# Kernel optimization log

Hardware: AMD Instinct MI355X
Metric: run time of the kernel (lower is better)

## Reference

```python
import jax, jax.numpy as jnp
import numpy as np
import math

N_STFT = 1025
N_MELS = 128
SAMPLE_RATE = 16000
F_MIN = 0.0
F_MAX = 8000.0
MAX_ITER = 20
LR = 0.3
MOMENTUM = 0.9
BATCH = 4
TIME = 1024


def _create_fb_matrix(n_freqs, f_min, f_max, n_mels, sample_rate):
    # Triangular mel filterbank, (n_freqs, n_mels), matching torchaudio's create_fb_matrix.
    all_freqs = np.linspace(0.0, sample_rate // 2, n_freqs)
    m_min = 2595.0 * math.log10(1.0 + f_min / 700.0)
    m_max = 2595.0 * math.log10(1.0 + f_max / 700.0)
    m_pts = np.linspace(m_min, m_max, n_mels + 2)
    f_pts = 700.0 * (10.0 ** (m_pts / 2595.0) - 1.0)
    f_diff = f_pts[1:] - f_pts[:-1]
    slopes = f_pts[None, :] - all_freqs[:, None]  # (n_freqs, n_mels+2)
    down_slopes = -slopes[:, :-2] / f_diff[:-1]
    up_slopes = slopes[:, 2:] / f_diff[1:]
    fb = np.maximum(0.0, np.minimum(down_slopes, up_slopes))
    return jnp.asarray(fb, dtype=jnp.float32)


def setup_inputs() -> dict:
    key = jax.random.key(0)
    k1, k2 = jax.random.split(key)
    melspec = jax.random.uniform(k1, (BATCH, N_MELS, TIME), dtype=jnp.float32)
    # torch.rand initialization of the estimated spectrogram, exposed for determinism
    spec_init = jax.random.uniform(k2, (BATCH, TIME, N_STFT), dtype=jnp.float32)
    fb = _create_fb_matrix(N_STFT, F_MIN, F_MAX, N_MELS, SAMPLE_RATE)
    return {"melspec": melspec, "spec_init": spec_init, "fb": fb}


def reference(melspec, spec_init, fb):
    # melspec: (B, n_mels, T) -> (B, T, n_mels); fb: (n_stft, n_mels)
    mel_t = jnp.swapaxes(melspec, -1, -2)
    b, t, _ = mel_t.shape
    inv = 2.0 / (b * t)  # d(mean over B*T of sum_m diff^2)/d(spec) prefactor

    def step(carry, _):
        spec, buf = carry
        diff = mel_t - jnp.einsum('btf,fm->btm', spec, fb)      # (B,T,M)
        grad = -inv * jnp.einsum('btm,fm->btf', diff, fb)       # (B,T,F)
        buf = MOMENTUM * buf + grad                              # SGD momentum buffer
        spec = jnp.maximum(spec - LR * buf, 0.0)                 # update + clamp(min=0)
        return (spec, buf), None

    init = (spec_init, jnp.zeros_like(spec_init))
    (spec, _), _ = jax.lax.scan(step, init, None, length=MAX_ITER)
    return jnp.swapaxes(spec, -1, -2)  # (B, n_stft, T)
```

## Files before the change

### kernel.cpp

```cpp
#include <hip/hip_runtime.h>

#define N_STFT 1025
#define N_MELS 128
#define BATCH 4
#define TIME 1024
#define MAX_ITER 20

typedef unsigned int u32;

__global__ void imel_prep(const float* __restrict__ fb, int* __restrict__ m0f,
                          float* __restrict__ w0a, float* __restrict__ w1a) {
  const int w = threadIdx.x >> 6, l = threadIdx.x & 63;
  const int f = blockIdx.x * 4 + w;
  if (f >= N_STFT) return;
  const float* row = fb + (size_t)f * N_MELS;
  const unsigned long long mlo = __ballot(row[l] != 0.0f);
  const unsigned long long mhi = __ballot(row[l + 64] != 0.0f);
  if (l == 0) {
    int m0 = mlo ? __builtin_ctzll(mlo)
                 : (mhi ? 64 + __builtin_ctzll(mhi) : 0);
    if (m0 > N_MELS - 2) m0 = N_MELS - 2;
    m0f[f] = m0;
    w0a[f] = row[m0];
    w1a[f] = row[m0 + 1];
  }
}

__global__ __launch_bounds__(256)
__attribute__((amdgpu_waves_per_eu(2, 4))) void imel_main(
    const float* __restrict__ melspec, const float* __restrict__ spec_init,
    const int* __restrict__ m0f, const float* __restrict__ w0a,
    const float* __restrict__ w1a, float* __restrict__ out) {
  __shared__ u32   s_P[4][N_MELS];
  __shared__ float s_mel[4][N_MELS];
  __shared__ float s_out[4][1060];

  const int tid = threadIdx.x;
  const int w   = tid >> 6;
  const int l   = tid & 63;
  const int flat = (blockIdx.x & 7) * 128 + (blockIdx.x >> 3);
  const int b   = flat >> 8;
  const int t0  = (flat & 255) << 2;
  const int tA  = t0 + w;

  for (int i = tid; i < 4 * N_MELS; i += 256) {
    const int m = i >> 2, r = i & 3;
    s_mel[r][m] = melspec[((size_t)b * N_MELS + m) * TIME + t0 + r];
  }
  __syncthreads();

  const float SCALE = 16777216.0f;
  const float SC48  = 281474976710656.0f;
  const float LRI48 = 5.2041704279304213e-19f;

  float rs[16], rb[16], rw0[16], rw1[16], cc[16];
  int rm[16];

  const float* srow = spec_init + (size_t)(b * TIME + tA) * N_STFT;
  const float* melW = &s_mel[w][0];
#pragma unroll
  for (int k = 0; k < 16; ++k) {
    const int f = (l << 4) + k;
    rs[k] = srow[f];
    const int m = m0f[f];
    rm[k] = m;
    const float w0 = w0a[f], w1 = w1a[f];
    rw0[k] = w0 * SCALE;
    rw1[k] = w1 * SCALE;
    cc[k] = -SC48 * fmaf(melW[m], w0, melW[m + 1] * w1);
    rb[k] = 0.f;
  }
  const float rt = (l == 63) ? srow[1024] : 0.f;

  u32* __restrict__ Pw = &s_P[w][0];
  Pw[l] = 0u;
  Pw[l + 64] = 0u;

  for (int it = 0; it < MAX_ITER; ++it) {
#pragma unroll
    for (int k = 0; k < 16; ++k) {
      const u32 v0 = (u32)fmaf(rs[k], rw0[k], 0.5f);
      const u32 v1 = (u32)fmaf(rs[k], rw1[k], 0.5f);
      atomicAdd(&Pw[rm[k]], v0);
      atomicAdd(&Pw[rm[k] + 1], v1);
    }
    __builtin_amdgcn_wave_barrier();
#pragma unroll
    for (int k = 0; k < 16; ++k) {
      const float p0 = (float)(int)Pw[rm[k]];
      const float p1 = (float)(int)Pw[rm[k] + 1];
      const float g  = fmaf(p1, rw1[k], fmaf(p0, rw0[k], cc[k]));
      rb[k] = fmaf(0.9f, rb[k], g);
      rs[k] = fmaxf(fmaf(-LRI48, rb[k], rs[k]), 0.f);
    }
    __builtin_amdgcn_wave_barrier();
    Pw[l] = 0u;
    Pw[l + 64] = 0u;
    __builtin_amdgcn_wave_barrier();
  }

#pragma unroll
  for (int k = 0; k < 16; ++k) {
    const int f = (l << 4) + k;
    s_out[w][f + (f >> 5)] = rs[k];
  }
  if (l == 63) s_out[w][1056] = rt;
  __syncthreads();

  const int tl = tid & 3;
  const int fg = tid >> 2;
  float* obase = out + (size_t)b * N_STFT * TIME + t0 + tl;
  for (int f = fg; f < N_STFT; f += 64) {
    obase[(size_t)f * TIME] = s_out[tl][f + (f >> 5)];
  }
}

extern "C" void kernel_launch(void* const* d_in, const int* in_sizes, int n_in,
                              void* d_out, int out_size, void* d_ws, size_t ws_size,
                              hipStream_t stream) {
  const float* melspec = (const float*)d_in[0];
  const float* spec_init = (const float*)d_in[1];
  const float* fb = (const float*)d_in[2];
  float* out = (float*)d_out;

  int* m0f = (int*)d_ws;
  float* w0a = (float*)((char*)d_ws + 5120);
  float* w1a = (float*)((char*)d_ws + 10240);

  imel_prep<<<dim3(257), dim3(256), 0, stream>>>(fb, m0f, w0a, w1a);
  imel_main<<<dim3(1024), dim3(256), 0, stream>>>(melspec, spec_init, m0f, w0a, w1a, out);
}
```

Measured before the change: 129.7 us.

## Pre-reduce per-lane mel contributions before LDS atomics and pad accumulator layout

New measurement: 124.4 us. 4.1% less time.

```diff
diff --git a/kernel.cpp b/kernel.cpp
--- a/kernel.cpp
+++ b/kernel.cpp
@@ -7,6 +7,7 @@
 #define MAX_ITER 20
 
 typedef unsigned int u32;
+typedef unsigned long long u64;
 
 __global__ void imel_prep(const float* __restrict__ fb, int* __restrict__ m0f,
                           float* __restrict__ w0a, float* __restrict__ w1a) {
@@ -31,7 +32,7 @@
     const float* __restrict__ melspec, const float* __restrict__ spec_init,
     const int* __restrict__ m0f, const float* __restrict__ w0a,
     const float* __restrict__ w1a, float* __restrict__ out) {
-  __shared__ u32   s_P[4][N_MELS];
+  __shared__ u32   s_P[4][136];
   __shared__ float s_mel[4][N_MELS];
   __shared__ float s_out[4][1060];
 
@@ -54,7 +55,7 @@
   const float LRI48 = 5.2041704279304213e-19f;
 
   float rs[16], rb[16], rw0[16], rw1[16], cc[16];
-  int rm[16];
+  int byA[16], byB[16];
 
   const float* srow = spec_init + (size_t)(b * TIME + tA) * N_STFT;
   const float* melW = &s_mel[w][0];
@@ -63,7 +64,8 @@
     const int f = (l << 4) + k;
     rs[k] = srow[f];
     const int m = m0f[f];
-    rm[k] = m;
+    byA[k] = (m + (m >> 5)) * 4;
+    byB[k] = ((m + 1) + ((m + 1) >> 5)) * 4;
     const float w0 = w0a[f], w1 = w1a[f];
     rw0[k] = w0 * SCALE;
     rw1[k] = w1 * SCALE;
@@ -72,30 +74,42 @@
   }
   const float rt = (l == 63) ? srow[1024] : 0.f;
 
-  u32* __restrict__ Pw = &s_P[w][0];
-  Pw[l] = 0u;
-  Pw[l + 64] = 0u;
+  char* __restrict__ Pw = (char*)&s_P[w][0];
+  {
+    u64* Pz = (u64*)Pw;
+    Pz[l] = 0ULL;
+    if (l < 4) Pz[64 + l] = 0ULL;
+  }
 
   for (int it = 0; it < MAX_ITER; ++it) {
+    {
+      float a0 = rs[0] * rw0[0], a1 = rs[0] * rw1[0];
 #pragma unroll
-    for (int k = 0; k < 16; ++k) {
-      const u32 v0 = (u32)fmaf(rs[k], rw0[k], 0.5f);
-      const u32 v1 = (u32)fmaf(rs[k], rw1[k], 0.5f);
-      atomicAdd(&Pw[rm[k]], v0);
-      atomicAdd(&Pw[rm[k] + 1], v1);
+      for (int k = 1; k < 16; ++k) {
+        const bool adv = (byA[k] != byA[k - 1]);
+        if (adv) atomicAdd((u32*)(Pw + byA[k - 1]), (u32)(a0 + 0.5f));
+        const float n0 = (adv ? a1 : a0) + rs[k] * rw0[k];
+        a1 = (adv ? 0.f : a1) + rs[k] * rw1[k];
+        a0 = n0;
+      }
+      atomicAdd((u32*)(Pw + byA[15]), (u32)(a0 + 0.5f));
+      atomicAdd((u32*)(Pw + byB[15]), (u32)(a1 + 0.5f));
     }
     __builtin_amdgcn_wave_barrier();
 #pragma unroll
     for (int k = 0; k < 16; ++k) {
-      const float p0 = (float)(int)Pw[rm[k]];
-      const float p1 = (float)(int)Pw[rm[k] + 1];
+      const float p0 = (float)(int)*(const u32*)(Pw + byA[k]);
+      const float p1 = (float)(int)*(const u32*)(Pw + byB[k]);
       const float g  = fmaf(p1, rw1[k], fmaf(p0, rw0[k], cc[k]));
       rb[k] = fmaf(0.9f, rb[k], g);
       rs[k] = fmaxf(fmaf(-LRI48, rb[k], rs[k]), 0.f);
     }
     __builtin_amdgcn_wave_barrier();
-    Pw[l] = 0u;
-    Pw[l + 64] = 0u;
+    {
+      u64* Pz = (u64*)Pw;
+      Pz[l] = 0ULL;
+      if (l < 4) Pz[64 + l] = 0ULL;
+    }
     __builtin_amdgcn_wave_barrier();
   }
 
```
